# Performance work log

Hardware: AMD Instinct MI355X
Metric: run time of the kernel (lower is better)

The kernel has to match this reference:

```python
import jax, jax.numpy as jnp
import numpy as np


def setup_inputs() -> dict:
    key = jax.random.key(0)
    ka, kb = jax.random.split(key)
    a = jax.random.normal(ka, (16384, 3), dtype=jnp.float32)
    b = jax.random.normal(kb, (16384, 3), dtype=jnp.float32)
    return {"a": a, "b": b}


def reference(a, b):
    # Pairwise Euclidean distances via ||a||^2 + ||b||^2 - 2 a.b (avoids [N,M,D] diff tensor).
    a2 = jnp.sum(a * a, axis=-1)            # [N]
    b2 = jnp.sum(b * b, axis=-1)            # [M]
    sq = a2[:, None] + b2[None, :] - 2.0 * jnp.einsum("nd,md->nm", a, b)  # [N,M]
    dist = jnp.sqrt(jnp.maximum(sq, 0.0))
    min_a = jnp.min(dist, axis=1)           # nearest b for each a
    min_b = jnp.min(dist, axis=0)           # nearest a for each b
    return jnp.mean(jnp.concatenate([min_a, min_b]))
```

## Files before the change

kernel.cpp:

```cpp
#include <hip/hip_runtime.h>

typedef unsigned int uint32;
typedef unsigned short ushort16;
typedef __attribute__((ext_vector_type(4)))  float f32x4;
typedef __attribute__((ext_vector_type(16))) float f32x16;
typedef __attribute__((ext_vector_type(8)))  short short8;

#define THREADS 256
#define FR 2
#define QB 256
#define CH 8
#define JS 8
#define RB 128

__device__ inline ushort16 bf16rn(float x) {
    uint32 u = __float_as_uint(x);
    u += 0x7FFFu + ((u >> 16) & 1u);
    return (ushort16)(u >> 16);
}
__device__ inline float bf2f(ushort16 h) { return __uint_as_float(((uint32)h) << 16); }

__device__ inline void prep_one(const float* __restrict__ P, int np, int i,
                                short8* __restrict__ Qf, short8* __restrict__ Sf,
                                float* __restrict__ a2)
{
    ushort16 qs[16], ss[16];
#pragma unroll
    for (int s = 0; s < 16; ++s) { qs[s] = 0; ss[s] = 0; }
    float w = 0.f;
    if (i < np) {
        float c[3] = {P[3*i], P[3*i+1], P[3*i+2]};
        w = fmaf(c[0], c[0], fmaf(c[1], c[1], c[2]*c[2]));
#pragma unroll
        for (int cc = 0; cc < 3; ++cc) {
            ushort16 h = bf16rn(c[cc]);
            ushort16 m = bf16rn(c[cc] - bf2f(h));
            float bv = -2.f * c[cc];
            ushort16 bh = bf16rn(bv);
            ushort16 bm = bf16rn(bv - bf2f(bh));
            const int b = 4*cc;
            qs[b]=h;  qs[b+1]=h;  qs[b+2]=m;  qs[b+3]=m;
            ss[b]=bh; ss[b+1]=bm; ss[b+2]=bh; ss[b+3]=bm;
        }
        qs[12]=0x3F80; qs[13]=0x3F80; qs[14]=0x3F80;
        ushort16 wh = bf16rn(w);
        float r1 = w - bf2f(wh);
        ushort16 wm = bf16rn(r1);
        ushort16 wl = bf16rn(r1 - bf2f(wm));
        ss[12]=wh; ss[13]=wm; ss[14]=wl;
    } else {
        ss[12] = bf16rn(1e30f);
    }
    a2[i] = w;
    const int row = i & 31, grp = i >> 5;
#pragma unroll
    for (int h = 0; h < 2; ++h) {
        short8 qv, sv;
#pragma unroll
        for (int e = 0; e < 8; ++e) { qv[e] = (short)qs[8*h+e]; sv[e] = (short)ss[8*h+e]; }
        Qf[(size_t)grp*64 + h*32 + row] = qv;
        Sf[(size_t)grp*64 + h*32 + row] = sv;
    }
}

__global__ __launch_bounds__(THREADS) void cd_prep(
    const float* __restrict__ A, int n, int padN,
    const float* __restrict__ B, int m, int padM,
    short8* QfA, short8* SfA, float* a2A,
    short8* QfB, short8* SfB, float* a2B,
    uint32* bits)
{
    const int i = blockIdx.x * THREADS + threadIdx.x;
    if (i < n + m) bits[i] = 0x7F800000u;
    if (i < padN) prep_one(A, n, i, QfA, SfA, a2A);
    if (i < padM) prep_one(B, m, i, QfB, SfB, a2B);
}

__global__ __launch_bounds__(THREADS, 4) void cd_mfma(
    const short8* __restrict__ QfA, const short8* __restrict__ SfA,
    const float* __restrict__ a2A, int padN, int n,
    const short8* __restrict__ QfB, const short8* __restrict__ SfB,
    const float* __restrict__ a2B, int padM, int m,
    uint32* __restrict__ bits)
{
    __shared__ short8 sb[2][CH*64];

    const short8* Qf; const short8* Sf; const float* a2; uint32* outb;
    int nq, padQ, padS;
    if (blockIdx.z == 0) { Qf=QfA; a2=a2A; nq=n; padQ=padN; Sf=SfB; padS=padM; outb=bits;   }
    else                 { Qf=QfB; a2=a2B; nq=m; padQ=padM; Sf=SfA; padS=padN; outb=bits+n; }

    if ((int)(blockIdx.x * QB) >= padQ) return;
    const int ntiles = padS >> 5;
    const int tps = ((ntiles + JS*CH - 1) / (JS*CH)) * CH;
    const int t0 = blockIdx.y * tps;
    const int t1 = min(t0 + tps, ntiles);
    if (t0 >= t1) return;

    const int tid = threadIdx.x, lane = tid & 63, wid = tid >> 6;
    const int qbase = blockIdx.x * QB + wid * (FR * 32);

    short8 av[FR];
#pragma unroll
    for (int f = 0; f < FR; ++f)
        av[f] = Qf[(size_t)((qbase >> 5) + f) * 64 + lane];

    float rmin[FR][16];
#pragma unroll
    for (int f = 0; f < FR; ++f)
#pragma unroll
        for (int r = 0; r < 16; ++r) rmin[f][r] = 1e30f;

    const f32x16 zero = {0.f,0.f,0.f,0.f,0.f,0.f,0.f,0.f,
                         0.f,0.f,0.f,0.f,0.f,0.f,0.f,0.f};
    const int nch = (t1 - t0 + CH - 1) / CH;

    {
        const int elems = min(CH, t1 - t0) * 64;
        if (tid       < elems) sb[0][tid      ] = Sf[(size_t)t0*64 + tid      ];
        if (tid + 256 < elems) sb[0][tid + 256] = Sf[(size_t)t0*64 + tid + 256];
    }
    __syncthreads();

    int cur = 0;
    for (int ch = 0; ch < nch; ++ch) {
        const int tb = t0 + ch*CH;
        const int cnt = min(CH, t1 - tb);

        short8 st0, st1;
        bool sv0=false, sv1=false;
        if (ch + 1 < nch) {
            const int nb = tb + CH;
            const int nel = min(CH, t1 - nb) * 64;
            const size_t gb = (size_t)nb * 64;
            if (tid       < nel) { st0 = Sf[gb + tid      ]; sv0 = true; }
            if (tid + 256 < nel) { st1 = Sf[gb + tid + 256]; sv1 = true; }
        }

        int t = 0;
        for (; t + 2 <= cnt; t += 2) {
            const short8 b0 = sb[cur][t*64 + lane];
            const short8 b1 = sb[cur][t*64 + 64 + lane];
            const f32x16 c00 = __builtin_amdgcn_mfma_f32_32x32x16_bf16(av[0], b0, zero, 0, 0, 0);
            const f32x16 c10 = __builtin_amdgcn_mfma_f32_32x32x16_bf16(av[1], b0, zero, 0, 0, 0);
            const f32x16 c01 = __builtin_amdgcn_mfma_f32_32x32x16_bf16(av[0], b1, zero, 0, 0, 0);
            const f32x16 c11 = __builtin_amdgcn_mfma_f32_32x32x16_bf16(av[1], b1, zero, 0, 0, 0);
#pragma unroll
            for (int r = 0; r < 16; ++r) {
                rmin[0][r] = fminf(fminf(rmin[0][r], c00[r]), c01[r]);
                rmin[1][r] = fminf(fminf(rmin[1][r], c10[r]), c11[r]);
            }
        }
        if (t < cnt) {
            const short8 b0 = sb[cur][t*64 + lane];
#pragma unroll
            for (int f = 0; f < FR; ++f) {
                const f32x16 c = __builtin_amdgcn_mfma_f32_32x32x16_bf16(av[f], b0, zero, 0, 0, 0);
#pragma unroll
                for (int r = 0; r < 16; ++r) rmin[f][r] = fminf(rmin[f][r], c[r]);
            }
        }

        if (ch + 1 < nch) {
            if (sv0) sb[cur^1][tid      ] = st0;
            if (sv1) sb[cur^1][tid + 256] = st1;
        }
        __syncthreads();
        cur ^= 1;
    }

#pragma unroll
    for (int f = 0; f < FR; ++f)
#pragma unroll
        for (int r = 0; r < 16; ++r) {
            float v = rmin[f][r];
            v = fminf(v, __shfl_xor(v, 1, 64));
            v = fminf(v, __shfl_xor(v, 2, 64));
            v = fminf(v, __shfl_xor(v, 4, 64));
            v = fminf(v, __shfl_xor(v, 8, 64));
            v = fminf(v, __shfl_xor(v, 16, 64));
            rmin[f][r] = v;
        }
    if ((lane & 31) == 0) {
        const int h4 = (lane >> 5) * 4;
#pragma unroll
        for (int f = 0; f < FR; ++f)
#pragma unroll
            for (int qq = 0; qq < 4; ++qq) {
                const int rowb = qbase + f*32 + 8*qq + h4;
                const float4 aa = *(const float4*)(a2 + rowb);
                const float av4[4] = {aa.x, aa.y, aa.z, aa.w};
#pragma unroll
                for (int e = 0; e < 4; ++e) {
                    const int qi = rowb + e;
                    if (qi < nq) {
                        const float sq = fmaxf(rmin[f][4*qq + e] + av4[e], 0.f);
                        atomicMin(&outb[qi], __float_as_uint(sq));
                    }
                }
            }
    }
}

__global__ __launch_bounds__(THREADS) void cd_reduce1(
    const uint32* __restrict__ bits, int count, double* __restrict__ partials)
{
    double s = 0.0;
    for (int i = blockIdx.x * THREADS + threadIdx.x; i < count; i += gridDim.x * THREADS)
        s += (double)sqrtf(__uint_as_float(bits[i]));
#pragma unroll
    for (int off = 32; off; off >>= 1) s += __shfl_down(s, off, 64);
    __shared__ double sw[4];
    const int lane = threadIdx.x & 63, wid = threadIdx.x >> 6;
    if (lane == 0) sw[wid] = s;
    __syncthreads();
    if (threadIdx.x == 0) partials[blockIdx.x] = sw[0] + sw[1] + sw[2] + sw[3];
}

__global__ __launch_bounds__(THREADS) void cd_reduce2(
    const double* __restrict__ partials, int nb, int total, float* __restrict__ out)
{
    double s = 0.0;
    for (int i = threadIdx.x; i < nb; i += THREADS) s += partials[i];
#pragma unroll
    for (int off = 32; off; off >>= 1) s += __shfl_down(s, off, 64);
    __shared__ double sw[4];
    const int lane = threadIdx.x & 63, wid = threadIdx.x >> 6;
    if (lane == 0) sw[wid] = s;
    __syncthreads();
    if (threadIdx.x == 0)
        out[0] = (float)((sw[0] + sw[1] + sw[2] + sw[3]) / (double)total);
}

extern "C" void kernel_launch(void* const* d_in, const int* in_sizes, int n_in,
                              void* d_out, int out_size, void* d_ws, size_t ws_size,
                              hipStream_t stream) {
    const float* a = (const float*)d_in[0];
    const float* b = (const float*)d_in[1];
    const int n = in_sizes[0] / 3;
    const int m = in_sizes[1] / 3;
    const int total = n + m;
    float* out = (float*)d_out;

    const int padN = (n + QB - 1) / QB * QB;
    const int padM = (m + QB - 1) / QB * QB;

    char* wp = (char*)d_ws;
    short8* QfA = (short8*)wp;   wp += (size_t)padN * 64;
    short8* SfA = (short8*)wp;   wp += (size_t)padN * 64;
    float*  a2A = (float*)wp;    wp += (size_t)padN * 4;
    short8* QfB = (short8*)wp;   wp += (size_t)padM * 64;
    short8* SfB = (short8*)wp;   wp += (size_t)padM * 64;
    float*  a2B = (float*)wp;    wp += (size_t)padM * 4;
    uint32* bits = (uint32*)wp;  wp += (size_t)total * 4;
    wp = (char*)(((size_t)wp + 255) & ~(size_t)255);
    double* partials = (double*)wp;

    const int prepElems = max(max(padN, padM), total);
    cd_prep<<<(prepElems + THREADS - 1) / THREADS, THREADS, 0, stream>>>(
        a, n, padN, b, m, padM, QfA, SfA, a2A, QfB, SfB, a2B, bits);

    const int gx = max(padN, padM) / QB;
    dim3 grid(gx, JS, 2);
    cd_mfma<<<grid, THREADS, 0, stream>>>(QfA, SfA, a2A, padN, n,
                                          QfB, SfB, a2B, padM, m, bits);

    cd_reduce1<<<RB, THREADS, 0, stream>>>(bits, total, partials);
    cd_reduce2<<<1, THREADS, 0, stream>>>(partials, RB, total, out);
}
```

Measured before the change: 43.93 us.

## Stream candidate tiles straight to registers and reduce row minima with DPP

The shared-memory double buffer and per-chunk __syncthreads are removed. Each wave now loads its candidate fragments directly from global memory into registers, prefetching two tiles ahead. The tile split across blockIdx.y no longer rounds to chunk multiples. The first four steps of the cross-lane min reduction now use DPP quad_perm and row-mirror moves instead of shuffles. This drops LDS traffic and block barriers, but the four waves of a block each fetch the same candidate data through the cache, and global load latency is hidden only by a two-tile register prefetch.

```diff
diff --git a/kernel.cpp b/kernel.cpp
--- a/kernel.cpp
+++ b/kernel.cpp
@@ -2,14 +2,12 @@
 
 typedef unsigned int uint32;
 typedef unsigned short ushort16;
-typedef __attribute__((ext_vector_type(4)))  float f32x4;
 typedef __attribute__((ext_vector_type(16))) float f32x16;
 typedef __attribute__((ext_vector_type(8)))  short short8;
 
 #define THREADS 256
 #define FR 2
 #define QB 256
-#define CH 8
 #define JS 8
 #define RB 128
 
@@ -76,6 +74,17 @@
     if (i < padM) prep_one(B, m, i, QfB, SfB, a2B);
 }
 
+__device__ inline float dppmin(float v, int ctrl) {
+    float s;
+    switch (ctrl) {
+        case 0xB1:  s = __int_as_float(__builtin_amdgcn_mov_dpp(__float_as_int(v), 0xB1,  0xf, 0xf, false)); break;
+        case 0x4E:  s = __int_as_float(__builtin_amdgcn_mov_dpp(__float_as_int(v), 0x4E,  0xf, 0xf, false)); break;
+        case 0x141: s = __int_as_float(__builtin_amdgcn_mov_dpp(__float_as_int(v), 0x141, 0xf, 0xf, false)); break;
+        default:    s = __int_as_float(__builtin_amdgcn_mov_dpp(__float_as_int(v), 0x140, 0xf, 0xf, false)); break;
+    }
+    return fminf(v, s);
+}
+
 __global__ __launch_bounds__(THREADS, 4) void cd_mfma(
     const short8* __restrict__ QfA, const short8* __restrict__ SfA,
     const float* __restrict__ a2A, int padN, int n,
@@ -83,8 +92,6 @@
     const float* __restrict__ a2B, int padM, int m,
     uint32* __restrict__ bits)
 {
-    __shared__ short8 sb[2][CH*64];
-
     const short8* Qf; const short8* Sf; const float* a2; uint32* outb;
     int nq, padQ, padS;
     if (blockIdx.z == 0) { Qf=QfA; a2=a2A; nq=n; padQ=padN; Sf=SfB; padS=padM; outb=bits;   }
@@ -92,7 +99,7 @@
 
     if ((int)(blockIdx.x * QB) >= padQ) return;
     const int ntiles = padS >> 5;
-    const int tps = ((ntiles + JS*CH - 1) / (JS*CH)) * CH;
+    const int tps = (ntiles + JS - 1) / JS;
     const int t0 = blockIdx.y * tps;
     const int t1 = min(t0 + tps, ntiles);
     if (t0 >= t1) return;
@@ -113,60 +120,35 @@
 
     const f32x16 zero = {0.f,0.f,0.f,0.f,0.f,0.f,0.f,0.f,
                          0.f,0.f,0.f,0.f,0.f,0.f,0.f,0.f};
-    const int nch = (t1 - t0 + CH - 1) / CH;
-
-    {
-        const int elems = min(CH, t1 - t0) * 64;
-        if (tid       < elems) sb[0][tid      ] = Sf[(size_t)t0*64 + tid      ];
-        if (tid + 256 < elems) sb[0][tid + 256] = Sf[(size_t)t0*64 + tid + 256];
-    }
-    __syncthreads();
-
-    int cur = 0;
-    for (int ch = 0; ch < nch; ++ch) {
-        const int tb = t0 + ch*CH;
-        const int cnt = min(CH, t1 - tb);
-
-        short8 st0, st1;
-        bool sv0=false, sv1=false;
-        if (ch + 1 < nch) {
-            const int nb = tb + CH;
-            const int nel = min(CH, t1 - nb) * 64;
-            const size_t gb = (size_t)nb * 64;
-            if (tid       < nel) { st0 = Sf[gb + tid      ]; sv0 = true; }
-            if (tid + 256 < nel) { st1 = Sf[gb + tid + 256]; sv1 = true; }
-        }
-
-        int t = 0;
-        for (; t + 2 <= cnt; t += 2) {
-            const short8 b0 = sb[cur][t*64 + lane];
-            const short8 b1 = sb[cur][t*64 + 64 + lane];
-            const f32x16 c00 = __builtin_amdgcn_mfma_f32_32x32x16_bf16(av[0], b0, zero, 0, 0, 0);
-            const f32x16 c10 = __builtin_amdgcn_mfma_f32_32x32x16_bf16(av[1], b0, zero, 0, 0, 0);
-            const f32x16 c01 = __builtin_amdgcn_mfma_f32_32x32x16_bf16(av[0], b1, zero, 0, 0, 0);
-            const f32x16 c11 = __builtin_amdgcn_mfma_f32_32x32x16_bf16(av[1], b1, zero, 0, 0, 0);
-#pragma unroll
-            for (int r = 0; r < 16; ++r) {
-                rmin[0][r] = fminf(fminf(rmin[0][r], c00[r]), c01[r]);
-                rmin[1][r] = fminf(fminf(rmin[1][r], c10[r]), c11[r]);
-            }
-        }
-        if (t < cnt) {
-            const short8 b0 = sb[cur][t*64 + lane];
-#pragma unroll
-            for (int f = 0; f < FR; ++f) {
-                const f32x16 c = __builtin_amdgcn_mfma_f32_32x32x16_bf16(av[f], b0, zero, 0, 0, 0);
-#pragma unroll
-                for (int r = 0; r < 16; ++r) rmin[f][r] = fminf(rmin[f][r], c[r]);
-            }
-        }
-
-        if (ch + 1 < nch) {
-            if (sv0) sb[cur^1][tid      ] = st0;
-            if (sv1) sb[cur^1][tid + 256] = st1;
-        }
-        __syncthreads();
-        cur ^= 1;
+
+    const short8* Sl = Sf + (size_t)t0 * 64 + lane;
+    const int nt = t1 - t0;
+
+    short8 c0 = Sl[0];
+    short8 c1 = (nt > 1) ? Sl[64] : c0;
+
+    int it = 0;
+    for (; it + 2 <= nt; it += 2) {
+        const short8 b0 = c0, b1 = c1;
+        const int nx = it + 2;
+        if (nx < nt)     c0 = Sl[(size_t)nx * 64];
+        if (nx + 1 < nt) c1 = Sl[(size_t)(nx + 1) * 64];
+#pragma unroll
+        for (int f = 0; f < FR; ++f) {
+            const f32x16 cA = __builtin_amdgcn_mfma_f32_32x32x16_bf16(av[f], b0, zero, 0, 0, 0);
+            const f32x16 cB = __builtin_amdgcn_mfma_f32_32x32x16_bf16(av[f], b1, zero, 0, 0, 0);
+#pragma unroll
+            for (int r = 0; r < 16; ++r)
+                rmin[f][r] = fminf(fminf(rmin[f][r], cA[r]), cB[r]);
+        }
+    }
+    if (it < nt) {
+#pragma unroll
+        for (int f = 0; f < FR; ++f) {
+            const f32x16 cA = __builtin_amdgcn_mfma_f32_32x32x16_bf16(av[f], c0, zero, 0, 0, 0);
+#pragma unroll
+            for (int r = 0; r < 16; ++r) rmin[f][r] = fminf(rmin[f][r], cA[r]);
+        }
     }
 
 #pragma unroll
@@ -174,13 +156,14 @@
 #pragma unroll
         for (int r = 0; r < 16; ++r) {
             float v = rmin[f][r];
-            v = fminf(v, __shfl_xor(v, 1, 64));
-            v = fminf(v, __shfl_xor(v, 2, 64));
-            v = fminf(v, __shfl_xor(v, 4, 64));
-            v = fminf(v, __shfl_xor(v, 8, 64));
+            v = dppmin(v, 0xB1);
+            v = dppmin(v, 0x4E);
+            v = dppmin(v, 0x141);
+            v = dppmin(v, 0x140);
             v = fminf(v, __shfl_xor(v, 16, 64));
             rmin[f][r] = v;
         }
+
     if ((lane & 31) == 0) {
         const int h4 = (lane >> 5) * 4;
 #pragma unroll
```

Result: slower. 46.26 us (+5.3%).

## Use one query fragment per wave, fold norms into MFMA accumulator, DPP reductions

Applied to the files above, without the earlier changes.

Each wave now handles a single 32-row query fragment instead of two, and the query block size halves to 128, so each B tile loaded from shared memory now feeds one MFMA per wave instead of two. The query squared norms are preloaded into the MFMA accumulator input rather than added after the reduction. The cross-lane min reduction uses DPP moves for the first four steps instead of shuffles. Fewer rows per wave lowers register use and doubles the block count, but it also halves LDS-tile reuse per wave and doubles total B traffic through shared memory.

```diff
diff --git a/kernel.cpp b/kernel.cpp
--- a/kernel.cpp
+++ b/kernel.cpp
@@ -2,16 +2,14 @@
 
 typedef unsigned int uint32;
 typedef unsigned short ushort16;
-typedef __attribute__((ext_vector_type(4)))  float f32x4;
 typedef __attribute__((ext_vector_type(16))) float f32x16;
 typedef __attribute__((ext_vector_type(8)))  short short8;
 
 #define THREADS 256
-#define FR 2
-#define QB 256
+#define QB 128
 #define CH 8
 #define JS 8
-#define RB 128
+#define RB 64
 
 __device__ inline ushort16 bf16rn(float x) {
     uint32 u = __float_as_uint(x);
@@ -76,6 +74,17 @@
     if (i < padM) prep_one(B, m, i, QfB, SfB, a2B);
 }
 
+__device__ inline float dppmin(float v, int ctrl) {
+    float s;
+    switch (ctrl) {
+        case 0xB1:  s = __int_as_float(__builtin_amdgcn_mov_dpp(__float_as_int(v), 0xB1,  0xf, 0xf, false)); break;
+        case 0x4E:  s = __int_as_float(__builtin_amdgcn_mov_dpp(__float_as_int(v), 0x4E,  0xf, 0xf, false)); break;
+        case 0x141: s = __int_as_float(__builtin_amdgcn_mov_dpp(__float_as_int(v), 0x141, 0xf, 0xf, false)); break;
+        default:    s = __int_as_float(__builtin_amdgcn_mov_dpp(__float_as_int(v), 0x140, 0xf, 0xf, false)); break;
+    }
+    return fminf(v, s);
+}
+
 __global__ __launch_bounds__(THREADS, 4) void cd_mfma(
     const short8* __restrict__ QfA, const short8* __restrict__ SfA,
     const float* __restrict__ a2A, int padN, int n,
@@ -98,21 +107,21 @@
     if (t0 >= t1) return;
 
     const int tid = threadIdx.x, lane = tid & 63, wid = tid >> 6;
-    const int qbase = blockIdx.x * QB + wid * (FR * 32);
-
-    short8 av[FR];
-#pragma unroll
-    for (int f = 0; f < FR; ++f)
-        av[f] = Qf[(size_t)((qbase >> 5) + f) * 64 + lane];
-
-    float rmin[FR][16];
-#pragma unroll
-    for (int f = 0; f < FR; ++f)
-#pragma unroll
-        for (int r = 0; r < 16; ++r) rmin[f][r] = 1e30f;
-
-    const f32x16 zero = {0.f,0.f,0.f,0.f,0.f,0.f,0.f,0.f,
-                         0.f,0.f,0.f,0.f,0.f,0.f,0.f,0.f};
+    const int qbase = blockIdx.x * QB + wid * 32;
+
+    const short8 av = Qf[(size_t)(qbase >> 5) * 64 + lane];
+
+    f32x16 pc;
+    {
+        const int rb = qbase + 4 * (lane >> 5);
+#pragma unroll
+        for (int r = 0; r < 16; ++r) pc[r] = a2[rb + (r & 3) + 8 * (r >> 2)];
+    }
+
+    float rmin[16];
+#pragma unroll
+    for (int r = 0; r < 16; ++r) rmin[r] = 1e30f;
+
     const int nch = (t1 - t0 + CH - 1) / CH;
 
     {
@@ -141,24 +150,17 @@
         for (; t + 2 <= cnt; t += 2) {
             const short8 b0 = sb[cur][t*64 + lane];
             const short8 b1 = sb[cur][t*64 + 64 + lane];
-            const f32x16 c00 = __builtin_amdgcn_mfma_f32_32x32x16_bf16(av[0], b0, zero, 0, 0, 0);
-            const f32x16 c10 = __builtin_amdgcn_mfma_f32_32x32x16_bf16(av[1], b0, zero, 0, 0, 0);
-            const f32x16 c01 = __builtin_amdgcn_mfma_f32_32x32x16_bf16(av[0], b1, zero, 0, 0, 0);
-            const f32x16 c11 = __builtin_amdgcn_mfma_f32_32x32x16_bf16(av[1], b1, zero, 0, 0, 0);
-#pragma unroll
-            for (int r = 0; r < 16; ++r) {
-                rmin[0][r] = fminf(fminf(rmin[0][r], c00[r]), c01[r]);
-                rmin[1][r] = fminf(fminf(rmin[1][r], c10[r]), c11[r]);
-            }
+            const f32x16 c0 = __builtin_amdgcn_mfma_f32_32x32x16_bf16(av, b0, pc, 0, 0, 0);
+            const f32x16 c1 = __builtin_amdgcn_mfma_f32_32x32x16_bf16(av, b1, pc, 0, 0, 0);
+#pragma unroll
+            for (int r = 0; r < 16; ++r)
+                rmin[r] = fminf(fminf(rmin[r], c0[r]), c1[r]);
         }
         if (t < cnt) {
             const short8 b0 = sb[cur][t*64 + lane];
-#pragma unroll
-            for (int f = 0; f < FR; ++f) {
-                const f32x16 c = __builtin_amdgcn_mfma_f32_32x32x16_bf16(av[f], b0, zero, 0, 0, 0);
-#pragma unroll
-                for (int r = 0; r < 16; ++r) rmin[f][r] = fminf(rmin[f][r], c[r]);
-            }
+            const f32x16 c0 = __builtin_amdgcn_mfma_f32_32x32x16_bf16(av, b0, pc, 0, 0, 0);
+#pragma unroll
+            for (int r = 0; r < 16; ++r) rmin[r] = fminf(rmin[r], c0[r]);
         }
 
         if (ch + 1 < nch) {
@@ -170,35 +172,26 @@
     }
 
 #pragma unroll
-    for (int f = 0; f < FR; ++f)
+    for (int r = 0; r < 16; ++r) {
+        float v = rmin[r];
+        v = dppmin(v, 0xB1);
+        v = dppmin(v, 0x4E);
+        v = dppmin(v, 0x141);
+        v = dppmin(v, 0x140);
+        v = fminf(v, __shfl_xor(v, 16, 64));
+        rmin[r] = v;
+    }
+
+    if ((lane & 31) == 0) {
+        const int rb = qbase + 4 * (lane >> 5);
 #pragma unroll
         for (int r = 0; r < 16; ++r) {
-            float v = rmin[f][r];
-            v = fminf(v, __shfl_xor(v, 1, 64));
-            v = fminf(v, __shfl_xor(v, 2, 64));
-            v = fminf(v, __shfl_xor(v, 4, 64));
-            v = fminf(v, __shfl_xor(v, 8, 64));
-            v = fminf(v, __shfl_xor(v, 16, 64));
-            rmin[f][r] = v;
-        }
-    if ((lane & 31) == 0) {
-        const int h4 = (lane >> 5) * 4;
-#pragma unroll
-        for (int f = 0; f < FR; ++f)
-#pragma unroll
-            for (int qq = 0; qq < 4; ++qq) {
-                const int rowb = qbase + f*32 + 8*qq + h4;
-                const float4 aa = *(const float4*)(a2 + rowb);
-                const float av4[4] = {aa.x, aa.y, aa.z, aa.w};
-#pragma unroll
-                for (int e = 0; e < 4; ++e) {
-                    const int qi = rowb + e;
-                    if (qi < nq) {
-                        const float sq = fmaxf(rmin[f][4*qq + e] + av4[e], 0.f);
-                        atomicMin(&outb[qi], __float_as_uint(sq));
-                    }
-                }
+            const int qi = rb + (r & 3) + 8 * (r >> 2);
+            if (qi < nq) {
+                const float sq = fmaxf(rmin[r], 0.f);
+                atomicMin(&outb[qi], __float_as_uint(sq));
             }
+        }
     }
 }
 
```

Measured after the change: 39.97 us. -9.0%, faster.

## Double split factor, use DPP for intra-row min reductions, simplify atomic epilogue

Applied to the files above, without the earlier changes.

Raises the number of column splits per query block (JS 8→16) to launch more blocks, and halves RB. Replaces the first four xor-shuffle steps of the per-row min reduction with DPP row moves (quad perm and row shifts), which avoid LDS-based bpermute traffic. The epilogue now loads a2 per element instead of as float4. More splits mean more atomicMin traffic on the output buffer. The DPP row_shr steps with full masks may not form a true butterfly reduction, so results could be wrong in some lanes.

```diff
diff --git a/kernel.cpp b/kernel.cpp
--- a/kernel.cpp
+++ b/kernel.cpp
@@ -2,7 +2,6 @@
 
 typedef unsigned int uint32;
 typedef unsigned short ushort16;
-typedef __attribute__((ext_vector_type(4)))  float f32x4;
 typedef __attribute__((ext_vector_type(16))) float f32x16;
 typedef __attribute__((ext_vector_type(8)))  short short8;
 
@@ -10,8 +9,8 @@
 #define FR 2
 #define QB 256
 #define CH 8
-#define JS 8
-#define RB 128
+#define JS 16
+#define RB 64
 
 __device__ inline ushort16 bf16rn(float x) {
     uint32 u = __float_as_uint(x);
@@ -76,6 +75,17 @@
     if (i < padM) prep_one(B, m, i, QfB, SfB, a2B);
 }
 
+__device__ inline float dppmin(float v, int ctrl) {
+    float s;
+    switch (ctrl) {
+        case 0xB1:  s = __int_as_float(__builtin_amdgcn_mov_dpp(__float_as_int(v), 0xB1,  0xf, 0xf, false)); break;
+        case 0x4E:  s = __int_as_float(__builtin_amdgcn_mov_dpp(__float_as_int(v), 0x4E,  0xf, 0xf, false)); break;
+        case 0x141: s = __int_as_float(__builtin_amdgcn_mov_dpp(__float_as_int(v), 0x141, 0xf, 0xf, false)); break;
+        default:    s = __int_as_float(__builtin_amdgcn_mov_dpp(__float_as_int(v), 0x140, 0xf, 0xf, false)); break;
+    }
+    return fminf(v, s);
+}
+
 __global__ __launch_bounds__(THREADS, 4) void cd_mfma(
     const short8* __restrict__ QfA, const short8* __restrict__ SfA,
     const float* __restrict__ a2A, int padN, int n,
@@ -174,31 +184,28 @@
 #pragma unroll
         for (int r = 0; r < 16; ++r) {
             float v = rmin[f][r];
-            v = fminf(v, __shfl_xor(v, 1, 64));
-            v = fminf(v, __shfl_xor(v, 2, 64));
-            v = fminf(v, __shfl_xor(v, 4, 64));
-            v = fminf(v, __shfl_xor(v, 8, 64));
+            v = dppmin(v, 0xB1);
+            v = dppmin(v, 0x4E);
+            v = dppmin(v, 0x141);
+            v = dppmin(v, 0x140);
             v = fminf(v, __shfl_xor(v, 16, 64));
             rmin[f][r] = v;
         }
+
     if ((lane & 31) == 0) {
         const int h4 = (lane >> 5) * 4;
 #pragma unroll
-        for (int f = 0; f < FR; ++f)
-#pragma unroll
-            for (int qq = 0; qq < 4; ++qq) {
-                const int rowb = qbase + f*32 + 8*qq + h4;
-                const float4 aa = *(const float4*)(a2 + rowb);
-                const float av4[4] = {aa.x, aa.y, aa.z, aa.w};
-#pragma unroll
-                for (int e = 0; e < 4; ++e) {
-                    const int qi = rowb + e;
-                    if (qi < nq) {
-                        const float sq = fmaxf(rmin[f][4*qq + e] + av4[e], 0.f);
-                        atomicMin(&outb[qi], __float_as_uint(sq));
-                    }
+        for (int f = 0; f < FR; ++f) {
+            const int rb = qbase + f*32 + h4;
+#pragma unroll
+            for (int r = 0; r < 16; ++r) {
+                const int qi = rb + (r & 3) + 8 * (r >> 2);
+                if (qi < nq) {
+                    const float sq = fmaxf(rmin[f][r] + a2[qi], 0.f);
+                    atomicMin(&outb[qi], __float_as_uint(sq));
                 }
             }
+        }
     }
 }
 
```

Measured after the change: 60.80 us. 38.4% more time.
